# Optimization experiments

Hardware: AMD Instinct MI355X
Metric: run time of the kernel (lower is better)

Reference implementation:

```python
import jax, jax.numpy as jnp
import numpy as np

IMAGE = 800.0
HIGH_THRESH = 0.7   # torchvision RPN fg_iou_thresh
LOW_THRESH = 0.3    # torchvision RPN bg_iou_thresh
BELOW_LOW = -1      # Matcher.BELOW_LOW_THRESHOLD
BETWEEN = -2        # Matcher.BETWEEN_THRESHOLDS


def _make_boxes(key, shape, max_wh):
    # shape = (..., 4) target; build valid xyxy boxes inside the image
    k1, k2 = jax.random.split(key)
    xy = jax.random.uniform(k1, shape[:-1] + (2,)) * (IMAGE - max_wh)
    wh = jax.random.uniform(k2, shape[:-1] + (2,)) * (max_wh - 4.0) + 4.0
    return jnp.concatenate([xy, xy + wh], axis=-1)


def setup_inputs() -> dict:
    key = jax.random.key(0)
    kA, kG, kS, kC = jax.random.split(key, 4)
    B, A, G = 4, 160000, 64
    anchors = _make_boxes(kA, (B, A, 4), 128.0)
    gt_boxes = _make_boxes(kG, (B, G, 4), 200.0)
    # soft score labels in {0, 0.5, 1} style: mostly 1, some <1 (ignored), some 0
    u = jax.random.uniform(kS, (B, G))
    score_labels = jnp.where(u < 0.15, 0.0, jnp.where(u < 0.3, 0.5, 1.0)).astype(jnp.float32)
    confidence_labels = jax.random.randint(kC, (B, G), 0, 2).astype(jnp.int32)
    return {"anchors": anchors, "gt_boxes": gt_boxes,
            "score_labels": score_labels, "confidence_labels": confidence_labels}


def _box_iou(a, b):
    # a: [G,4] gt, b: [A,4] anchors -> [G,A]
    area_a = (a[:, 2] - a[:, 0]) * (a[:, 3] - a[:, 1])          # [G]
    area_b = (b[:, 2] - b[:, 0]) * (b[:, 3] - b[:, 1])          # [A]
    lt = jnp.maximum(a[:, None, :2], b[None, :, :2])            # [G,A,2]
    rb = jnp.minimum(a[:, None, 2:], b[None, :, 2:])            # [G,A,2]
    wh = jnp.clip(rb - lt, 0.0)
    inter = wh[..., 0] * wh[..., 1]                              # [G,A]
    return inter / (area_a[:, None] + area_b[None, :] - inter)


def _matcher(mq):
    # torchvision Matcher with allow_low_quality_matches=True. mq: [G,A]
    matched_vals = mq.max(axis=0)                                # [A]
    matches = mq.argmax(axis=0).astype(jnp.int32)                # [A]
    m = jnp.where(matched_vals < LOW_THRESH, BELOW_LOW,
                  jnp.where(matched_vals < HIGH_THRESH, BETWEEN, matches))
    # restore, for each gt, anchors achieving that gt's max IoU
    highest_per_gt = mq.max(axis=1, keepdims=True)               # [G,1]
    low_quality = (mq == highest_per_gt).any(axis=0)             # [A]
    return jnp.where(low_quality, matches, m)


def _assign_one(anchors, gt, scores, confs):
    mq = _box_iou(gt, anchors)                                   # [G,A]
    midx = _matcher(mq)                                          # [A]
    cl = jnp.clip(midx, 0)
    matched_gt = gt[cl]                                          # [A,4]
    pos = midx >= 0
    labels = pos.astype(jnp.float32)
    labels = jnp.minimum(labels, scores[cl])
    labels = jnp.where(midx == BELOW_LOW, 0.0, labels)
    labels = jnp.where(midx == BETWEEN, -1.0, labels)
    labels = jnp.where((scores[cl] < 1.0) & pos, -1.0, labels)
    labels = jnp.where((confs[cl] == 0) & pos, -1.0, labels)
    return labels, matched_gt


def reference(anchors, gt_boxes, score_labels, confidence_labels):
    labels, matched_gt_boxes = jax.vmap(_assign_one)(anchors, gt_boxes, score_labels, confidence_labels)
    return labels, matched_gt_boxes
```

## Files before the change

### kernel.cpp

```cpp
#include <hip/hip_runtime.h>

constexpr int NB = 4;
constexpr int NA = 160000;
constexpr int NG = 64;

__device__ __forceinline__ float box_area(float x0, float y0, float x1, float y1) {
#pragma clang fp contract(off)
    return (x1 - x0) * (y1 - y0);
}

__device__ __forceinline__ float iou_f(float gx0, float gy0, float gx1, float gy1, float garea,
                                       float ax0, float ay0, float ax1, float ay1, float aarea) {
#pragma clang fp contract(off)
    float ltx = fmaxf(gx0, ax0);
    float lty = fmaxf(gy0, ay0);
    float rbx = fminf(gx1, ax1);
    float rby = fminf(gy1, ay1);
    float w = fmaxf(rbx - ltx, 0.0f);
    float h = fmaxf(rby - lty, 0.0f);
    float inter = w * h;
    float s = garea + aarea;
    float denom = s - inter;
    return inter / denom;
}

__global__ __launch_bounds__(256) void k_gt_highest(
        const float* __restrict__ anchors, const float* __restrict__ gts,
        float* __restrict__ highest ) {
    const int b = blockIdx.y;
    const int lane = threadIdx.x & 63;
    const int wid = __builtin_amdgcn_readfirstlane(threadIdx.x >> 6);

    const float4* __restrict__ gt4 = reinterpret_cast<const float4*>(gts) + b * NG;
    const float4* __restrict__ anc = reinterpret_cast<const float4*>(anchors) + (size_t)b * NA;

    float4 g = gt4[lane];
    float garea = box_area(g.x, g.y, g.z, g.w);

    const int base = blockIdx.x * 640 + wid * 160;
    float acc = 0.0f;
#pragma unroll 8
    for (int i = 0; i < 160; ++i) {
        float4 a = anc[base + i];
        float aarea = box_area(a.x, a.y, a.z, a.w);
        float v = iou_f(g.x, g.y, g.z, g.w, garea,
                        a.x, a.y, a.z, a.w, aarea);
        acc = fmaxf(acc, v);
    }

    __shared__ float part[4][NG];
    part[wid][lane] = acc;
    __syncthreads();
    if (threadIdx.x < NG) {
        float m = fmaxf(fmaxf(part[0][threadIdx.x], part[1][threadIdx.x]),
                        fmaxf(part[2][threadIdx.x], part[3][threadIdx.x]));
        atomicMax(reinterpret_cast<int*>(&highest[b * NG + threadIdx.x]),
                  __float_as_int(m));
    }
}

__global__ __launch_bounds__(256) void k_assign(
        const float* __restrict__ anchors, const float* __restrict__ gts,
        const float* __restrict__ scores, const int* __restrict__ confs,
        const float* __restrict__ highest,
        float* __restrict__ labels_out, float4* __restrict__ boxes_out) {
    __shared__ float4 sg[NG];
    __shared__ float sga[NG], shi[NG], ssc[NG];
    __shared__ int scf[NG];

    const int b = blockIdx.y;
    if (threadIdx.x < NG) {
        const int gi = threadIdx.x;
        float4 gv = reinterpret_cast<const float4*>(gts)[b * NG + gi];
        sg[gi] = gv;
        sga[gi] = box_area(gv.x, gv.y, gv.z, gv.w);
        shi[gi] = highest[b * NG + gi];
        ssc[gi] = scores[b * NG + gi];
        scf[gi] = confs[b * NG + gi];
    }
    __syncthreads();

    const int ai = blockIdx.x * 256 + threadIdx.x;
    const float4* __restrict__ anc = reinterpret_cast<const float4*>(anchors) + (size_t)b * NA;
    float4 av = anc[ai];
    float aarea = box_area(av.x, av.y, av.z, av.w);

    float best = -1.0f;
    int   matches = 0;
    bool  lowq = false;
#pragma unroll
    for (int g = 0; g < NG; ++g) {
        float4 gb = sg[g];
        float v = iou_f(gb.x, gb.y, gb.z, gb.w, sga[g],
                        av.x, av.y, av.z, av.w, aarea);
        if (v > best) { best = v; matches = g; }
        lowq |= (v == shi[g]);
    }

    int m    = (best < 0.3f) ? -1 : ((best < 0.7f) ? -2 : matches);
    int midx = lowq ? matches : m;
    int cl   = (midx < 0) ? 0 : midx;

    float4 mg = sg[cl];
    float  sc = ssc[cl];
    int    cf = scf[cl];

    bool pos = (midx >= 0);
    float lab = pos ? 1.0f : 0.0f;
    lab = fminf(lab, sc);
    if (midx == -1) lab = 0.0f;
    if (midx == -2) lab = -1.0f;
    if (sc < 1.0f && pos) lab = -1.0f;
    if (cf == 0 && pos) lab = -1.0f;

    labels_out[(size_t)b * NA + ai] = lab;
    boxes_out[(size_t)b * NA + ai] = mg;
}

extern "C" void kernel_launch(void* const* d_in, const int* in_sizes, int n_in,
                              void* d_out, int out_size, void* d_ws, size_t ws_size,
                              hipStream_t stream) {
    const float* anchors = (const float*)d_in[0];
    const float* gts     = (const float*)d_in[1];
    const float* scores  = (const float*)d_in[2];
    const int*   confs   = (const int*)d_in[3];

    float* labels_out = (float*)d_out;
    float4* boxes_out = (float4*)((float*)d_out + (size_t)NB * NA);
    float* highest = (float*)d_ws;

    hipMemsetAsync(d_ws, 0, (size_t)NB * NG * sizeof(float), stream);

    dim3 g1(250, NB), g2(625, NB), blk(256);
    k_gt_highest<<<g1, blk, 0, stream>>>(anchors, gts, highest);
    k_assign<<<g2, blk, 0, stream>>>(anchors, gts, scores, confs, highest,
                                     labels_out, boxes_out);
}
```

Baseline: 153.3 us.

## Defer IoU division via fraction compare and process two anchors per thread

The per-GT max kernel now tracks the best intersection/denominator pair and compares candidates by double-precision cross multiplication, dividing only once per wave partial. This removes a float division from the inner loop. It also splits the anchor range into four times as many blocks with 40 anchors per wave. The assign kernel uses 128-thread blocks where each thread handles two anchors, so each shared GT load is reused across both. Double-precision multiplies are slow on some hardware and may offset the saved divides.

```diff
diff --git a/kernel.cpp b/kernel.cpp
--- a/kernel.cpp
+++ b/kernel.cpp
@@ -9,8 +9,9 @@
     return (x1 - x0) * (y1 - y0);
 }
 
-__device__ __forceinline__ float iou_f(float gx0, float gy0, float gx1, float gy1, float garea,
-                                       float ax0, float ay0, float ax1, float ay1, float aarea) {
+__device__ __forceinline__ void inter_denom(float gx0, float gy0, float gx1, float gy1, float garea,
+                                            float ax0, float ay0, float ax1, float ay1, float aarea,
+                                            float& inter, float& denom) {
 #pragma clang fp contract(off)
     float ltx = fmaxf(gx0, ax0);
     float lty = fmaxf(gy0, ay0);
@@ -18,10 +19,20 @@
     float rby = fminf(gy1, ay1);
     float w = fmaxf(rbx - ltx, 0.0f);
     float h = fmaxf(rby - lty, 0.0f);
-    float inter = w * h;
+    inter = w * h;
     float s = garea + aarea;
-    float denom = s - inter;
+    denom = s - inter;
+}
+
+__device__ __forceinline__ float iou_f(float gx0, float gy0, float gx1, float gy1, float garea,
+                                       float ax0, float ay0, float ax1, float ay1, float aarea) {
+    float inter, denom;
+    inter_denom(gx0, gy0, gx1, gy1, garea, ax0, ay0, ax1, ay1, aarea, inter, denom);
     return inter / denom;
+}
+
+__device__ __forceinline__ bool frac_gt(float i1, float d1, float i2, float d2) {
+    return (double)i1 * (double)d2 > (double)i2 * (double)d1;
 }
 
 __global__ __launch_bounds__(256) void k_gt_highest(
@@ -37,29 +48,36 @@
     float4 g = gt4[lane];
     float garea = box_area(g.x, g.y, g.z, g.w);
 
-    const int base = blockIdx.x * 640 + wid * 160;
-    float acc = 0.0f;
+    const int base = blockIdx.x * 160 + wid * 40;
+    float bi = 0.0f, bd = 1.0f;
 #pragma unroll 8
-    for (int i = 0; i < 160; ++i) {
+    for (int i = 0; i < 40; ++i) {
         float4 a = anc[base + i];
         float aarea = box_area(a.x, a.y, a.z, a.w);
-        float v = iou_f(g.x, g.y, g.z, g.w, garea,
-                        a.x, a.y, a.z, a.w, aarea);
-        acc = fmaxf(acc, v);
+        float inter, denom;
+        inter_denom(g.x, g.y, g.z, g.w, garea, a.x, a.y, a.z, a.w, aarea,
+                    inter, denom);
+        if (frac_gt(inter, denom, bi, bd)) { bi = inter; bd = denom; }
     }
 
-    __shared__ float part[4][NG];
-    part[wid][lane] = acc;
+    __shared__ float pi[4][NG], pd[4][NG];
+    pi[wid][lane] = bi;
+    pd[wid][lane] = bd;
     __syncthreads();
     if (threadIdx.x < NG) {
-        float m = fmaxf(fmaxf(part[0][threadIdx.x], part[1][threadIdx.x]),
-                        fmaxf(part[2][threadIdx.x], part[3][threadIdx.x]));
+        float ci = pi[0][threadIdx.x], cd = pd[0][threadIdx.x];
+#pragma unroll
+        for (int wv = 1; wv < 4; ++wv) {
+            float ni = pi[wv][threadIdx.x], nd = pd[wv][threadIdx.x];
+            if (frac_gt(ni, nd, ci, cd)) { ci = ni; cd = nd; }
+        }
+        float m = ci / cd;
         atomicMax(reinterpret_cast<int*>(&highest[b * NG + threadIdx.x]),
                   __float_as_int(m));
     }
 }
 
-__global__ __launch_bounds__(256) void k_assign(
+__global__ __launch_bounds__(128) void k_assign(
         const float* __restrict__ anchors, const float* __restrict__ gts,
         const float* __restrict__ scores, const int* __restrict__ confs,
         const float* __restrict__ highest,
@@ -80,41 +98,59 @@
     }
     __syncthreads();
 
-    const int ai = blockIdx.x * 256 + threadIdx.x;
+    const int ai0 = blockIdx.x * 256 + threadIdx.x;
+    const int ai1 = ai0 + 128;
     const float4* __restrict__ anc = reinterpret_cast<const float4*>(anchors) + (size_t)b * NA;
-    float4 av = anc[ai];
-    float aarea = box_area(av.x, av.y, av.z, av.w);
+    float4 av0 = anc[ai0];
+    float4 av1 = anc[ai1];
+    float aarea0 = box_area(av0.x, av0.y, av0.z, av0.w);
+    float aarea1 = box_area(av1.x, av1.y, av1.z, av1.w);
 
-    float best = -1.0f;
-    int   matches = 0;
-    bool  lowq = false;
+    float best0 = -1.0f, best1 = -1.0f;
+    int   mat0 = 0, mat1 = 0;
+    bool  lowq0 = false, lowq1 = false;
 #pragma unroll
     for (int g = 0; g < NG; ++g) {
         float4 gb = sg[g];
-        float v = iou_f(gb.x, gb.y, gb.z, gb.w, sga[g],
-                        av.x, av.y, av.z, av.w, aarea);
-        if (v > best) { best = v; matches = g; }
-        lowq |= (v == shi[g]);
+        float ga = sga[g];
+        float hg = shi[g];
+        float v0 = iou_f(gb.x, gb.y, gb.z, gb.w, ga,
+                         av0.x, av0.y, av0.z, av0.w, aarea0);
+        float v1 = iou_f(gb.x, gb.y, gb.z, gb.w, ga,
+                         av1.x, av1.y, av1.z, av1.w, aarea1);
+        if (v0 > best0) { best0 = v0; mat0 = g; }
+        if (v1 > best1) { best1 = v1; mat1 = g; }
+        lowq0 |= (v0 == hg);
+        lowq1 |= (v1 == hg);
     }
 
-    int m    = (best < 0.3f) ? -1 : ((best < 0.7f) ? -2 : matches);
-    int midx = lowq ? matches : m;
-    int cl   = (midx < 0) ? 0 : midx;
+    const size_t obase = (size_t)b * NA;
+#pragma unroll
+    for (int k = 0; k < 2; ++k) {
+        float best = k ? best1 : best0;
+        int matches = k ? mat1 : mat0;
+        bool lowq = k ? lowq1 : lowq0;
+        int ai = k ? ai1 : ai0;
 
-    float4 mg = sg[cl];
-    float  sc = ssc[cl];
-    int    cf = scf[cl];
+        int m    = (best < 0.3f) ? -1 : ((best < 0.7f) ? -2 : matches);
+        int midx = lowq ? matches : m;
+        int cl   = (midx < 0) ? 0 : midx;
 
-    bool pos = (midx >= 0);
-    float lab = pos ? 1.0f : 0.0f;
-    lab = fminf(lab, sc);
-    if (midx == -1) lab = 0.0f;
-    if (midx == -2) lab = -1.0f;
-    if (sc < 1.0f && pos) lab = -1.0f;
-    if (cf == 0 && pos) lab = -1.0f;
+        float4 mg = sg[cl];
+        float  sc = ssc[cl];
+        int    cf = scf[cl];
 
-    labels_out[(size_t)b * NA + ai] = lab;
-    boxes_out[(size_t)b * NA + ai] = mg;
+        bool pos = (midx >= 0);
+        float lab = pos ? 1.0f : 0.0f;
+        lab = fminf(lab, sc);
+        if (midx == -1) lab = 0.0f;
+        if (midx == -2) lab = -1.0f;
+        if (sc < 1.0f && pos) lab = -1.0f;
+        if (cf == 0 && pos) lab = -1.0f;
+
+        labels_out[obase + ai] = lab;
+        boxes_out[obase + ai] = mg;
+    }
 }
 
 extern "C" void kernel_launch(void* const* d_in, const int* in_sizes, int n_in,
@@ -131,8 +167,8 @@
 
     hipMemsetAsync(d_ws, 0, (size_t)NB * NG * sizeof(float), stream);
 
-    dim3 g1(250, NB), g2(625, NB), blk(256);
-    k_gt_highest<<<g1, blk, 0, stream>>>(anchors, gts, highest);
-    k_assign<<<g2, blk, 0, stream>>>(anchors, gts, scores, confs, highest,
-                                     labels_out, boxes_out);
+    dim3 g1(1000, NB), g2(625, NB), blk1(256), blk2(128);
+    k_gt_highest<<<g1, blk1, 0, stream>>>(anchors, gts, highest);
+    k_assign<<<g2, blk2, 0, stream>>>(anchors, gts, scores, confs, highest,
+                                      labels_out, boxes_out);
 }
```

Measured after the change: 146.6 us. 4.4% less time.

## Defer IoU division in per-GT max via cross-multiplied fraction compare

Applied to the files above, without the earlier changes.

The per-GT max-IoU pass now tracks the best (inter, denom) pair and compares candidates by cross-multiplying in double precision, so it divides only once per wave result instead of once per anchor. The grid for that pass grows fourfold, with each wave covering 40 anchors instead of 160, to raise parallelism. The assign kernel packs GT area and highest IoU into one float2 shared load and unrolls the GT loop by 4 instead of fully. The risks are the cost of FP64 multiplies on the GPU and a possible change in tie-breaking when two fractions are compared exactly rather than their rounded quotients.

```diff
diff --git a/kernel.cpp b/kernel.cpp
--- a/kernel.cpp
+++ b/kernel.cpp
@@ -9,8 +9,9 @@
     return (x1 - x0) * (y1 - y0);
 }
 
-__device__ __forceinline__ float iou_f(float gx0, float gy0, float gx1, float gy1, float garea,
-                                       float ax0, float ay0, float ax1, float ay1, float aarea) {
+__device__ __forceinline__ void inter_denom(float gx0, float gy0, float gx1, float gy1, float garea,
+                                            float ax0, float ay0, float ax1, float ay1, float aarea,
+                                            float& inter, float& denom) {
 #pragma clang fp contract(off)
     float ltx = fmaxf(gx0, ax0);
     float lty = fmaxf(gy0, ay0);
@@ -18,10 +19,20 @@
     float rby = fminf(gy1, ay1);
     float w = fmaxf(rbx - ltx, 0.0f);
     float h = fmaxf(rby - lty, 0.0f);
-    float inter = w * h;
+    inter = w * h;
     float s = garea + aarea;
-    float denom = s - inter;
+    denom = s - inter;
+}
+
+__device__ __forceinline__ float iou_f(float gx0, float gy0, float gx1, float gy1, float garea,
+                                       float ax0, float ay0, float ax1, float ay1, float aarea) {
+    float inter, denom;
+    inter_denom(gx0, gy0, gx1, gy1, garea, ax0, ay0, ax1, ay1, aarea, inter, denom);
     return inter / denom;
+}
+
+__device__ __forceinline__ bool frac_gt(float i1, float d1, float i2, float d2) {
+    return (double)i1 * (double)d2 > (double)i2 * (double)d1;
 }
 
 __global__ __launch_bounds__(256) void k_gt_highest(
@@ -37,23 +48,30 @@
     float4 g = gt4[lane];
     float garea = box_area(g.x, g.y, g.z, g.w);
 
-    const int base = blockIdx.x * 640 + wid * 160;
-    float acc = 0.0f;
+    const int base = blockIdx.x * 160 + wid * 40;
+    float bi = 0.0f, bd = 1.0f;
 #pragma unroll 8
-    for (int i = 0; i < 160; ++i) {
+    for (int i = 0; i < 40; ++i) {
         float4 a = anc[base + i];
         float aarea = box_area(a.x, a.y, a.z, a.w);
-        float v = iou_f(g.x, g.y, g.z, g.w, garea,
-                        a.x, a.y, a.z, a.w, aarea);
-        acc = fmaxf(acc, v);
+        float inter, denom;
+        inter_denom(g.x, g.y, g.z, g.w, garea, a.x, a.y, a.z, a.w, aarea,
+                    inter, denom);
+        if (frac_gt(inter, denom, bi, bd)) { bi = inter; bd = denom; }
     }
 
-    __shared__ float part[4][NG];
-    part[wid][lane] = acc;
+    __shared__ float pi[4][NG], pd[4][NG];
+    pi[wid][lane] = bi;
+    pd[wid][lane] = bd;
     __syncthreads();
     if (threadIdx.x < NG) {
-        float m = fmaxf(fmaxf(part[0][threadIdx.x], part[1][threadIdx.x]),
-                        fmaxf(part[2][threadIdx.x], part[3][threadIdx.x]));
+        float ci = pi[0][threadIdx.x], cd = pd[0][threadIdx.x];
+#pragma unroll
+        for (int wv = 1; wv < 4; ++wv) {
+            float ni = pi[wv][threadIdx.x], nd = pd[wv][threadIdx.x];
+            if (frac_gt(ni, nd, ci, cd)) { ci = ni; cd = nd; }
+        }
+        float m = ci / cd;
         atomicMax(reinterpret_cast<int*>(&highest[b * NG + threadIdx.x]),
                   __float_as_int(m));
     }
@@ -65,7 +83,8 @@
         const float* __restrict__ highest,
         float* __restrict__ labels_out, float4* __restrict__ boxes_out) {
     __shared__ float4 sg[NG];
-    __shared__ float sga[NG], shi[NG], ssc[NG];
+    __shared__ float2 sah[NG];
+    __shared__ float ssc[NG];
     __shared__ int scf[NG];
 
     const int b = blockIdx.y;
@@ -73,8 +92,8 @@
         const int gi = threadIdx.x;
         float4 gv = reinterpret_cast<const float4*>(gts)[b * NG + gi];
         sg[gi] = gv;
-        sga[gi] = box_area(gv.x, gv.y, gv.z, gv.w);
-        shi[gi] = highest[b * NG + gi];
+        sah[gi] = make_float2(box_area(gv.x, gv.y, gv.z, gv.w),
+                              highest[b * NG + gi]);
         ssc[gi] = scores[b * NG + gi];
         scf[gi] = confs[b * NG + gi];
     }
@@ -88,13 +107,14 @@
     float best = -1.0f;
     int   matches = 0;
     bool  lowq = false;
-#pragma unroll
+#pragma unroll 4
     for (int g = 0; g < NG; ++g) {
         float4 gb = sg[g];
-        float v = iou_f(gb.x, gb.y, gb.z, gb.w, sga[g],
+        float2 ah = sah[g];
+        float v = iou_f(gb.x, gb.y, gb.z, gb.w, ah.x,
                         av.x, av.y, av.z, av.w, aarea);
         if (v > best) { best = v; matches = g; }
-        lowq |= (v == shi[g]);
+        lowq |= (v == ah.y);
     }
 
     int m    = (best < 0.3f) ? -1 : ((best < 0.7f) ? -2 : matches);
@@ -131,7 +151,7 @@
 
     hipMemsetAsync(d_ws, 0, (size_t)NB * NG * sizeof(float), stream);
 
-    dim3 g1(250, NB), g2(625, NB), blk(256);
+    dim3 g1(1000, NB), g2(625, NB), blk(256);
     k_gt_highest<<<g1, blk, 0, stream>>>(anchors, gts, highest);
     k_assign<<<g2, blk, 0, stream>>>(anchors, gts, scores, confs, highest,
                                      labels_out, boxes_out);
```

After: 142.7 us. -6.9%, faster.
